# Kernel tuning notes

Measured on AMD Instinct MI355X. Metric: run time of the kernel, lower is better.

The kernel has to match this reference:

```python
import jax, jax.numpy as jnp
import numpy as np

N_NODES = 100000
N_EDGES = 1000000
D_FEAT = 64


def setup_inputs() -> dict:
    key = jax.random.key(0)
    k1, k2, k3 = jax.random.split(key, 3)
    feature = jax.random.normal(k1, (N_NODES, D_FEAT), dtype=jnp.float32)
    src = jax.random.randint(k2, (N_EDGES,), 0, N_NODES, dtype=jnp.int64 if jax.config.jax_enable_x64 else jnp.int32)
    dst = jax.random.randint(k3, (N_EDGES,), 0, N_NODES, dtype=jnp.int64 if jax.config.jax_enable_x64 else jnp.int32)
    return {"feature": feature, "src": src, "dst": dst}


def reference(feature, src, dst):
    n = feature.shape[0]
    ones = jnp.ones(src.shape[0], dtype=feature.dtype)
    # out_degrees: edges leaving each node (src side); in_degrees: edges arriving (dst side)
    out_deg = jax.ops.segment_sum(ones, src, num_segments=n)
    in_deg = jax.ops.segment_sum(ones, dst, num_segments=n)
    norm_src = jnp.clip(out_deg, 1.0, None) ** -0.5  # [N]
    norm_dst = jnp.clip(in_deg, 1.0, None) ** -0.5   # [N]
    h = feature * norm_src[:, None]                  # pre-normalize
    msg = h[src]                                     # gather [E, D]
    agg = jax.ops.segment_sum(msg, dst, num_segments=n)  # scatter-sum [N, D]
    return agg * norm_dst[:, None]                   # post-normalize
```

## Files before the change

### kernel.cpp

```cpp
#include <hip/hip_runtime.h>

#define D_FEAT 64
#define NODE_CAP 131072
#define NCHUNK 32
#define NWORDS (NODE_CAP / 8)
#define SCAN_T 128
#define SCAN_BLOCKS (NWORDS / SCAN_T)

typedef float    f32x4 __attribute__((ext_vector_type(4)));
typedef _Float16 h16x8 __attribute__((ext_vector_type(8)));

__global__ void convert_kernel(const float* __restrict__ feat,
                               _Float16* __restrict__ feat16, int n8) {
    int i = blockIdx.x * blockDim.x + threadIdx.x;
    if (i >= n8) return;
    const f32x4* p = (const f32x4*)(feat + (size_t)i * 8);
    f32x4 a = p[0], b = p[1];
    h16x8 h;
    h[0] = (_Float16)a[0]; h[1] = (_Float16)a[1];
    h[2] = (_Float16)a[2]; h[3] = (_Float16)a[3];
    h[4] = (_Float16)b[0]; h[5] = (_Float16)b[1];
    h[6] = (_Float16)b[2]; h[7] = (_Float16)b[3];
    *(h16x8*)(feat16 + (size_t)i * 8) = h;
}

__global__ void __launch_bounds__(1024)
hist_kernel(const int* __restrict__ dst, const int* __restrict__ src,
            unsigned int* __restrict__ cnt_dst, unsigned int* __restrict__ cnt_src,
            unsigned char* __restrict__ rank, int* __restrict__ flags,
            int E, int cs) {
    __shared__ unsigned int h[NWORDS];
    if (blockIdx.x == 0 && threadIdx.x < 2 * SCAN_BLOCKS)
        flags[threadIdx.x] = 0;
    const bool is_src = (blockIdx.x >= NCHUNK);
    const int chunk = is_src ? blockIdx.x - NCHUNK : blockIdx.x;

    for (int i = threadIdx.x; i < NWORDS; i += blockDim.x) h[i] = 0;
    __syncthreads();

    const int e0 = chunk * cs;
    const int e1 = min(e0 + cs, E);
    if (e0 < e1) {
        const int nfull = (e1 - e0) & ~3;
        if (is_src) {
            for (int e = e0 + threadIdx.x * 4; e < e0 + nfull; e += blockDim.x * 4) {
                int4 v = *(const int4*)(src + e);
                atomicAdd(&h[(unsigned)v.x >> 3], 1u << (((unsigned)v.x & 7u) << 2));
                atomicAdd(&h[(unsigned)v.y >> 3], 1u << (((unsigned)v.y & 7u) << 2));
                atomicAdd(&h[(unsigned)v.z >> 3], 1u << (((unsigned)v.z & 7u) << 2));
                atomicAdd(&h[(unsigned)v.w >> 3], 1u << (((unsigned)v.w & 7u) << 2));
            }
            for (int e = e0 + nfull + threadIdx.x; e < e1; e += blockDim.x) {
                unsigned n = (unsigned)src[e];
                atomicAdd(&h[n >> 3], 1u << ((n & 7u) << 2));
            }
        } else {
            for (int e = e0 + threadIdx.x * 4; e < e0 + nfull; e += blockDim.x * 4) {
                int4 v = *(const int4*)(dst + e);
                unsigned sh, old; uchar4 r4;
                sh = ((unsigned)v.x & 7u) << 2;
                old = atomicAdd(&h[(unsigned)v.x >> 3], 1u << sh);
                r4.x = (unsigned char)((old >> sh) & 15u);
                sh = ((unsigned)v.y & 7u) << 2;
                old = atomicAdd(&h[(unsigned)v.y >> 3], 1u << sh);
                r4.y = (unsigned char)((old >> sh) & 15u);
                sh = ((unsigned)v.z & 7u) << 2;
                old = atomicAdd(&h[(unsigned)v.z >> 3], 1u << sh);
                r4.z = (unsigned char)((old >> sh) & 15u);
                sh = ((unsigned)v.w & 7u) << 2;
                old = atomicAdd(&h[(unsigned)v.w >> 3], 1u << sh);
                r4.w = (unsigned char)((old >> sh) & 15u);
                *(uchar4*)(rank + e) = r4;
            }
            for (int e = e0 + nfull + threadIdx.x; e < e1; e += blockDim.x) {
                unsigned n = (unsigned)dst[e];
                unsigned sh = (n & 7u) << 2;
                unsigned old = atomicAdd(&h[n >> 3], 1u << sh);
                rank[e] = (unsigned char)((old >> sh) & 15u);
            }
        }
    }
    __syncthreads();
    unsigned int* slab = (is_src ? cnt_src : cnt_dst) + (size_t)chunk * NWORDS;
    for (int i = threadIdx.x; i < NWORDS; i += blockDim.x) slab[i] = h[i];
}

__global__ void __launch_bounds__(SCAN_T)
scan_kernel(const unsigned int* __restrict__ cnt_dst,
            const unsigned int* __restrict__ cnt_src,
            unsigned long long* __restrict__ pre,
            int* __restrict__ row_start, int* __restrict__ deg_dst,
            float* __restrict__ coef_src,
            int* __restrict__ agg, int* __restrict__ incl) {
    __shared__ int lds[SCAN_T];
    __shared__ int s_prev;
    const int t = threadIdx.x;
    const int c = blockIdx.x;
    const int wi = c * SCAN_T + t;

    unsigned runE = 0, runO = 0;
    #pragma unroll 8
    for (int cc = 0; cc < NCHUNK; ++cc) {
        unsigned w = cnt_dst[(size_t)cc * NWORDS + wi];
        unsigned plo = __byte_perm(runE, runO, 0x5140);
        unsigned phi = __byte_perm(runE, runO, 0x7362);
        pre[(size_t)cc * NWORDS + wi] = ((unsigned long long)phi << 32) | plo;
        runE += w & 0x0F0F0F0Fu;
        runO += (w >> 4) & 0x0F0F0F0Fu;
    }
    unsigned oE = 0, oO = 0;
    #pragma unroll 8
    for (int cc = 0; cc < NCHUNK; ++cc) {
        unsigned w = cnt_src[(size_t)cc * NWORDS + wi];
        oE += w & 0x0F0F0F0Fu;
        oO += (w >> 4) & 0x0F0F0F0Fu;
    }
    const int d0 = runE & 255,         d1 = runO & 255;
    const int d2 = (runE >> 8) & 255,  d3 = (runO >> 8) & 255;
    const int d4 = (runE >> 16) & 255, d5 = (runO >> 16) & 255;
    const int d6 = runE >> 24,         d7 = runO >> 24;
    const int v = d0 + d1 + d2 + d3 + d4 + d5 + d6 + d7;
    lds[t] = v;
    __syncthreads();
    for (int off = 1; off < SCAN_T; off <<= 1) {
        int x = (t >= off) ? lds[t - off] : 0;
        __syncthreads();
        lds[t] += x;
        __syncthreads();
    }
    const int local_incl = lds[t];
    const int total      = lds[SCAN_T - 1];
    if (t == 0)
        __hip_atomic_store(&agg[c], total + 1, __ATOMIC_RELEASE, __HIP_MEMORY_SCOPE_AGENT);
    if (t < 64) {
        int prev = 0;
        if (c > 0) {
            int j = c - 1;
            while (true) {
                int idx = j - t;
                bool valid = (idx >= 0);
                int iv = 0, av = 0;
                if (valid) {
                    while (true) {
                        iv = __hip_atomic_load(&incl[idx], __ATOMIC_ACQUIRE,
                                               __HIP_MEMORY_SCOPE_AGENT);
                        if (iv) break;
                        if (idx > 0) {
                            av = __hip_atomic_load(&agg[idx], __ATOMIC_ACQUIRE,
                                                   __HIP_MEMORY_SCOPE_AGENT);
                            if (av) break;
                        }
                    }
                }
                unsigned long long m = __ballot(valid && (iv != 0));
                int contrib; bool done;
                if (m) {
                    int lstar = __ffsll((long long)m) - 1;
                    contrib = (t < lstar) ? (av - 1) : (t == lstar ? iv - 1 : 0);
                    done = true;
                } else {
                    contrib = valid ? (av - 1) : 0;
                    done = false;
                }
                #pragma unroll
                for (int off = 32; off >= 1; off >>= 1) contrib += __shfl_xor(contrib, off);
                prev += contrib;
                if (done) break;
                j -= 64;
            }
        }
        if (t == 0) {
            __hip_atomic_store(&incl[c], prev + total + 1, __ATOMIC_RELEASE,
                               __HIP_MEMORY_SCOPE_AGENT);
            s_prev = prev;
        }
    }
    __syncthreads();
    int run = s_prev + local_incl - v;
    const int g = wi * 8;
    int4 rs;
    rs.x = run; run += d0; rs.y = run; run += d1; rs.z = run; run += d2; rs.w = run; run += d3;
    *(int4*)(row_start + g) = rs;
    rs.x = run; run += d4; rs.y = run; run += d5; rs.z = run; run += d6; rs.w = run;
    *(int4*)(row_start + g + 4) = rs;
    *(int4*)(deg_dst + g)     = make_int4(d0, d1, d2, d3);
    *(int4*)(deg_dst + g + 4) = make_int4(d4, d5, d6, d7);
    float4 cf;
    cf.x = rsqrtf((float)max((int)(oE & 255), 1));
    cf.y = rsqrtf((float)max((int)(oO & 255), 1));
    cf.z = rsqrtf((float)max((int)((oE >> 8) & 255), 1));
    cf.w = rsqrtf((float)max((int)((oO >> 8) & 255), 1));
    *(float4*)(coef_src + g) = cf;
    cf.x = rsqrtf((float)max((int)((oE >> 16) & 255), 1));
    cf.y = rsqrtf((float)max((int)((oO >> 16) & 255), 1));
    cf.z = rsqrtf((float)max((int)(oE >> 24), 1));
    cf.w = rsqrtf((float)max((int)(oO >> 24), 1));
    *(float4*)(coef_src + g + 4) = cf;
}

__global__ void place_kernel(const int* __restrict__ src, const int* __restrict__ dst,
                             const unsigned char* __restrict__ rank,
                             const unsigned char* __restrict__ pre8,
                             const int* __restrict__ row_start,
                             int* __restrict__ edges, int E, int cs) {
    int e4 = (blockIdx.x * blockDim.x + threadIdx.x) * 4;
    if (e4 >= E) return;
    if (e4 + 3 < E) {
        int4 d4 = *(const int4*)(dst + e4);
        int4 s4 = *(const int4*)(src + e4);
        uchar4 r4 = *(const uchar4*)(rank + e4);
        const unsigned char* pc = pre8 + (size_t)(e4 / cs) * NODE_CAP;
        edges[row_start[d4.x] + (int)pc[d4.x] + (int)r4.x] = s4.x;
        edges[row_start[d4.y] + (int)pc[d4.y] + (int)r4.y] = s4.y;
        edges[row_start[d4.z] + (int)pc[d4.z] + (int)r4.z] = s4.z;
        edges[row_start[d4.w] + (int)pc[d4.w] + (int)r4.w] = s4.w;
    } else {
        for (int e = e4; e < E; ++e) {
            int d = dst[e];
            const unsigned char* pc = pre8 + (size_t)(e / cs) * NODE_CAP;
            edges[row_start[d] + (int)pc[d] + (int)rank[e]] = src[e];
        }
    }
}

__global__ void aggregate_kernel(const _Float16* __restrict__ feat16,
                                 const int* __restrict__ edges,
                                 const float* __restrict__ coef_src,
                                 const int* __restrict__ row_start,
                                 const int* __restrict__ deg_dst,
                                 float* __restrict__ out, int N) {
    int w = blockIdx.x * (blockDim.x >> 6) + (threadIdx.x >> 6);
    int lane = threadIdx.x & 63;
    int n0 = 2 * w;
    int n1 = 2 * w + 1;
    if (n0 >= N) return;
    int g = lane >> 3;
    int q = lane & 7;
    int k0 = deg_dst[n0], b0 = row_start[n0];
    int k1 = (n1 < N) ? deg_dst[n1] : 0;
    int b1 = (n1 < N) ? row_start[n1] : 0;

    f32x4 a0l = {0.f,0.f,0.f,0.f}, a0h = {0.f,0.f,0.f,0.f};
    f32x4 a1l = {0.f,0.f,0.f,0.f}, a1h = {0.f,0.f,0.f,0.f};
    int kmax = max(k0, k1);
    for (int i0 = 0; i0 < kmax; i0 += 64) {
        int e0 = 0, e1 = 0;
        float c0 = 0.f, c1 = 0.f;
        if (i0 + lane < k0) { e0 = edges[b0 + i0 + lane]; c0 = coef_src[e0]; }
        if (i0 + lane < k1) { e1 = edges[b1 + i0 + lane]; c1 = coef_src[e1]; }
        int kk = min(64, kmax - i0);
        for (int t8 = 0; t8 * 8 < kk; ++t8) {
            int ei = t8 * 8 + g;
            int   s0 = __shfl(e0, ei);
            float cc0 = __shfl(c0, ei);
            int   s1 = __shfl(e1, ei);
            float cc1 = __shfl(c1, ei);
            if (i0 + ei < k0) {
                h16x8 r = *(const h16x8*)(feat16 + (size_t)s0 * D_FEAT + q * 8);
                a0l[0] += (float)r[0] * cc0; a0l[1] += (float)r[1] * cc0;
                a0l[2] += (float)r[2] * cc0; a0l[3] += (float)r[3] * cc0;
                a0h[0] += (float)r[4] * cc0; a0h[1] += (float)r[5] * cc0;
                a0h[2] += (float)r[6] * cc0; a0h[3] += (float)r[7] * cc0;
            }
            if (i0 + ei < k1) {
                h16x8 r = *(const h16x8*)(feat16 + (size_t)s1 * D_FEAT + q * 8);
                a1l[0] += (float)r[0] * cc1; a1l[1] += (float)r[1] * cc1;
                a1l[2] += (float)r[2] * cc1; a1l[3] += (float)r[3] * cc1;
                a1h[0] += (float)r[4] * cc1; a1h[1] += (float)r[5] * cc1;
                a1h[2] += (float)r[6] * cc1; a1h[3] += (float)r[7] * cc1;
            }
        }
    }
    #pragma unroll
    for (int m = 8; m <= 32; m <<= 1) {
        #pragma unroll
        for (int j = 0; j < 4; ++j) {
            a0l[j] += __shfl_xor(a0l[j], m); a0h[j] += __shfl_xor(a0h[j], m);
            a1l[j] += __shfl_xor(a1l[j], m); a1h[j] += __shfl_xor(a1h[j], m);
        }
    }
    if (g == 0) {
        float nd0 = rsqrtf((float)max(k0, 1));
        a0l *= nd0; a0h *= nd0;
        f32x4* o0 = (f32x4*)(out + (size_t)n0 * D_FEAT + q * 8);
        __builtin_nontemporal_store(a0l, o0);
        __builtin_nontemporal_store(a0h, o0 + 1);
        if (n1 < N) {
            float nd1 = rsqrtf((float)max(k1, 1));
            a1l *= nd1; a1h *= nd1;
            f32x4* o1 = (f32x4*)(out + (size_t)n1 * D_FEAT + q * 8);
            __builtin_nontemporal_store(a1l, o1);
            __builtin_nontemporal_store(a1h, o1 + 1);
        }
    }
}

extern "C" void kernel_launch(void* const* d_in, const int* in_sizes, int n_in,
                              void* d_out, int out_size, void* d_ws, size_t ws_size,
                              hipStream_t stream) {
    const float* feat = (const float*)d_in[0];
    const int*   src  = (const int*)d_in[1];
    const int*   dst  = (const int*)d_in[2];
    float* out = (float*)d_out;

    const int E = in_sizes[1];
    const int N = in_sizes[0] / D_FEAT;

    const int cs = ((E + NCHUNK - 1) / NCHUNK + 3) & ~3;

    unsigned int* cnt_dst = (unsigned int*)d_ws;
    unsigned int* cnt_src = cnt_dst + (size_t)NCHUNK * NWORDS;
    unsigned long long* pre = (unsigned long long*)(cnt_src + (size_t)NCHUNK * NWORDS);
    int* row_start = (int*)(pre + (size_t)NCHUNK * NWORDS);
    int* deg_dst   = row_start + NODE_CAP;
    float* coef_src = (float*)(deg_dst + NODE_CAP);
    int* flags = (int*)(coef_src + NODE_CAP);
    _Float16* feat16 = (_Float16*)(flags + 2 * SCAN_BLOCKS);
    int* edges = (int*)(feat16 + (size_t)NODE_CAP * D_FEAT);
    unsigned char* rank = (unsigned char*)(edges + E);
    (void)ws_size;

    const int n8 = N * (D_FEAT / 8);
    convert_kernel<<<(n8 + 255) / 256, 256, 0, stream>>>(feat, feat16, n8);
    hist_kernel<<<2 * NCHUNK, 1024, 0, stream>>>(dst, src, cnt_dst, cnt_src,
                                                 rank, flags, E, cs);
    scan_kernel<<<SCAN_BLOCKS, SCAN_T, 0, stream>>>(cnt_dst, cnt_src, pre, row_start,
                                                    deg_dst, coef_src,
                                                    flags, flags + SCAN_BLOCKS);
    place_kernel<<<((E + 3) / 4 + 255) / 256, 256, 0, stream>>>(
        src, dst, rank, (const unsigned char*)pre, row_start, edges, E, cs);
    aggregate_kernel<<<(N + 7) / 8, 256, 0, stream>>>(feat16, edges, coef_src,
                                                      row_start, deg_dst, out, N);
}
```

Measured before the change: 158.2 us.

## Fuse fp16 conversion into histogram launch and batch gather loads in aggregation

The separate fp32-to-fp16 conversion kernel is folded into the histogram kernel as extra blocks, so conversion runs alongside the 64 histogram blocks and one launch is saved. The aggregation inner loop is fully unrolled into three phases (shuffles, eight independent 16-byte gathers per node, then accumulation) to raise memory-level parallelism. The unrolled form always processes 8 slots and zero-fills masked loads, and it uses more registers. Conversion blocks also reserve 64KB of static LDS they never use, which limits how many of them fit per CU.

```diff
diff --git a/kernel.cpp b/kernel.cpp
--- a/kernel.cpp
+++ b/kernel.cpp
@@ -6,30 +6,33 @@
 #define NWORDS (NODE_CAP / 8)
 #define SCAN_T 128
 #define SCAN_BLOCKS (NWORDS / SCAN_T)
+#define CONV_BLOCKS 256
 
 typedef float    f32x4 __attribute__((ext_vector_type(4)));
 typedef _Float16 h16x8 __attribute__((ext_vector_type(8)));
-
-__global__ void convert_kernel(const float* __restrict__ feat,
-                               _Float16* __restrict__ feat16, int n8) {
-    int i = blockIdx.x * blockDim.x + threadIdx.x;
-    if (i >= n8) return;
-    const f32x4* p = (const f32x4*)(feat + (size_t)i * 8);
-    f32x4 a = p[0], b = p[1];
-    h16x8 h;
-    h[0] = (_Float16)a[0]; h[1] = (_Float16)a[1];
-    h[2] = (_Float16)a[2]; h[3] = (_Float16)a[3];
-    h[4] = (_Float16)b[0]; h[5] = (_Float16)b[1];
-    h[6] = (_Float16)b[2]; h[7] = (_Float16)b[3];
-    *(h16x8*)(feat16 + (size_t)i * 8) = h;
-}
 
 __global__ void __launch_bounds__(1024)
 hist_kernel(const int* __restrict__ dst, const int* __restrict__ src,
             unsigned int* __restrict__ cnt_dst, unsigned int* __restrict__ cnt_src,
             unsigned char* __restrict__ rank, int* __restrict__ flags,
-            int E, int cs) {
+            const float* __restrict__ feat, _Float16* __restrict__ feat16,
+            int n8, int E, int cs) {
     __shared__ unsigned int h[NWORDS];
+    if (blockIdx.x >= 2 * NCHUNK) {
+        int i = (blockIdx.x - 2 * NCHUNK) * 1024 + threadIdx.x;
+        const int stride = CONV_BLOCKS * 1024;
+        for (; i < n8; i += stride) {
+            const f32x4* p = (const f32x4*)(feat + (size_t)i * 8);
+            f32x4 a = p[0], b = p[1];
+            h16x8 v;
+            v[0] = (_Float16)a[0]; v[1] = (_Float16)a[1];
+            v[2] = (_Float16)a[2]; v[3] = (_Float16)a[3];
+            v[4] = (_Float16)b[0]; v[5] = (_Float16)b[1];
+            v[6] = (_Float16)b[2]; v[7] = (_Float16)b[3];
+            *(h16x8*)(feat16 + (size_t)i * 8) = v;
+        }
+        return;
+    }
     if (blockIdx.x == 0 && threadIdx.x < 2 * SCAN_BLOCKS)
         flags[threadIdx.x] = 0;
     const bool is_src = (blockIdx.x >= NCHUNK);
@@ -248,27 +251,36 @@
         float c0 = 0.f, c1 = 0.f;
         if (i0 + lane < k0) { e0 = edges[b0 + i0 + lane]; c0 = coef_src[e0]; }
         if (i0 + lane < k1) { e1 = edges[b1 + i0 + lane]; c1 = coef_src[e1]; }
-        int kk = min(64, kmax - i0);
-        for (int t8 = 0; t8 * 8 < kk; ++t8) {
-            int ei = t8 * 8 + g;
-            int   s0 = __shfl(e0, ei);
-            float cc0 = __shfl(c0, ei);
-            int   s1 = __shfl(e1, ei);
-            float cc1 = __shfl(c1, ei);
-            if (i0 + ei < k0) {
-                h16x8 r = *(const h16x8*)(feat16 + (size_t)s0 * D_FEAT + q * 8);
-                a0l[0] += (float)r[0] * cc0; a0l[1] += (float)r[1] * cc0;
-                a0l[2] += (float)r[2] * cc0; a0l[3] += (float)r[3] * cc0;
-                a0h[0] += (float)r[4] * cc0; a0h[1] += (float)r[5] * cc0;
-                a0h[2] += (float)r[6] * cc0; a0h[3] += (float)r[7] * cc0;
-            }
-            if (i0 + ei < k1) {
-                h16x8 r = *(const h16x8*)(feat16 + (size_t)s1 * D_FEAT + q * 8);
-                a1l[0] += (float)r[0] * cc1; a1l[1] += (float)r[1] * cc1;
-                a1l[2] += (float)r[2] * cc1; a1l[3] += (float)r[3] * cc1;
-                a1h[0] += (float)r[4] * cc1; a1h[1] += (float)r[5] * cc1;
-                a1h[2] += (float)r[6] * cc1; a1h[3] += (float)r[7] * cc1;
-            }
+
+        int   s0r[8], s1r[8];
+        float c0r[8], c1r[8];
+        #pragma unroll
+        for (int t = 0; t < 8; ++t) {
+            int ei = t * 8 + g;
+            s0r[t] = __shfl(e0, ei); c0r[t] = __shfl(c0, ei);
+            s1r[t] = __shfl(e1, ei); c1r[t] = __shfl(c1, ei);
+        }
+        const h16x8 hz = {};
+        h16x8 r0[8], r1[8];
+        #pragma unroll
+        for (int t = 0; t < 8; ++t) {
+            int ei = t * 8 + g;
+            r0[t] = (i0 + ei < k0)
+                  ? *(const h16x8*)(feat16 + (size_t)s0r[t] * D_FEAT + q * 8) : hz;
+            r1[t] = (i0 + ei < k1)
+                  ? *(const h16x8*)(feat16 + (size_t)s1r[t] * D_FEAT + q * 8) : hz;
+        }
+        #pragma unroll
+        for (int t = 0; t < 8; ++t) {
+            float cc0 = c0r[t], cc1 = c1r[t];
+            a0l[0] += (float)r0[t][0] * cc0; a0l[1] += (float)r0[t][1] * cc0;
+            a0l[2] += (float)r0[t][2] * cc0; a0l[3] += (float)r0[t][3] * cc0;
+            a0h[0] += (float)r0[t][4] * cc0; a0h[1] += (float)r0[t][5] * cc0;
+            a0h[2] += (float)r0[t][6] * cc0; a0h[3] += (float)r0[t][7] * cc0;
+            a1l[0] += (float)r1[t][0] * cc1; a1l[1] += (float)r1[t][1] * cc1;
+            a1l[2] += (float)r1[t][2] * cc1; a1l[3] += (float)r1[t][3] * cc1;
+            a1h[0] += (float)r1[t][4] * cc1; a1h[1] += (float)r1[t][5] * cc1;
+            a1h[2] += (float)r1[t][6] * cc1; a1h[3] += (float)r1[t][7] * cc1;
         }
     }
     #pragma unroll
@@ -321,9 +333,8 @@
     (void)ws_size;
 
     const int n8 = N * (D_FEAT / 8);
-    convert_kernel<<<(n8 + 255) / 256, 256, 0, stream>>>(feat, feat16, n8);
-    hist_kernel<<<2 * NCHUNK, 1024, 0, stream>>>(dst, src, cnt_dst, cnt_src,
-                                                 rank, flags, E, cs);
+    hist_kernel<<<2 * NCHUNK + CONV_BLOCKS, 1024, 0, stream>>>(
+        dst, src, cnt_dst, cnt_src, rank, flags, feat, feat16, n8, E, cs);
     scan_kernel<<<SCAN_BLOCKS, SCAN_T, 0, stream>>>(cnt_dst, cnt_src, pre, row_start,
                                                     deg_dst, coef_src,
                                                     flags, flags + SCAN_BLOCKS);
```

After: 192.7 us. +21.8%, slower.
